# Optimization experiments

Measured on AMD Instinct MI355X. Metric: run time of the kernel, lower is better.

The kernel has to match this reference:

```python
import jax, jax.numpy as jnp
import numpy as np

EPS = 1e-6


def setup_inputs() -> dict:
    key = jax.random.key(0)
    k1, k2, k3, k4, k5, k6, k7 = jax.random.split(key, 7)
    B, S, D, P = 16384, 8, 128, 65536
    return {
        "z_samples": jax.random.normal(k1, (B, S, D), dtype=jnp.float32),
        "alpha": jax.random.normal(k2, (), dtype=jnp.float32),
        "beta": jax.random.normal(k3, (), dtype=jnp.float32),
        "ap": jax.random.randint(k4, (P,), 0, B),
        "p": jax.random.randint(k5, (P,), 0, B),
        "an": jax.random.randint(k6, (P,), 0, B),
        "n": jax.random.randint(k7, (P,), 0, B),
    }


def _pairwise_sqdist(Xa, Xb):
    # Xa, Xb: [P, S, D] -> d2: [P, S, S] where d2[p,i,j] = ||Xa[p,i]-Xb[p,j]||^2
    S = Xa.shape[1]
    rows = []
    for i in range(S):  # S is a small fixed constant (n_samples)
        diff = Xa[:, i, None, :] - Xb  # [P, S, D]
        rows.append(jnp.sum(diff * diff, axis=-1))  # [P, S]
    return jnp.stack(rows, axis=1)  # [P, S, S]


def reference(z_samples, alpha, beta, ap, p, an, n):
    S = z_samples.shape[1]
    a = jax.nn.softplus(alpha)
    d2_pos = _pairwise_sqdist(z_samples[ap], z_samples[p])  # [P, S, S]
    d2_neg = _pairwise_sqdist(z_samples[an], z_samples[n])  # [P, S, S]
    prob_pos = jax.nn.sigmoid(-a * d2_pos + beta) + EPS
    prob_neg = jax.nn.sigmoid(-a * d2_neg + beta) + EPS
    per_pair = jnp.sum(-jnp.log(prob_pos) - jnp.log(1.0 - prob_neg), axis=(1, 2))
    per_pair = per_pair / (S * S)
    return jnp.mean(per_pair)
```

## Files before the change

kernel.cpp:

```cpp
#include <hip/hip_runtime.h>


typedef __attribute__((ext_vector_type(8))) short bf16x8;
typedef __attribute__((ext_vector_type(4))) float f32x4;

#define EPS 1e-6f
#define BLOCK_THREADS 256
#define WAVES_PER_BLOCK (BLOCK_THREADS / 64)

__global__ __launch_bounds__(BLOCK_THREADS) void prep_kernel(
    const float* __restrict__ z,
    unsigned char* __restrict__ zq,
    float* __restrict__ norms,
    int totalChunks, int strideChunks)
{
    const int lane = threadIdx.x & 63;
    const int wv   = threadIdx.x >> 6;
    const int wave = blockIdx.x * WAVES_PER_BLOCK + wv;
    const int rg   = lane >> 4;
    const int part = lane & 15;

    for (int chunk = wave; chunk < totalChunks; chunk += strideChunks) {
        const size_t rowBase = (size_t)chunk * 4;
        const size_t off = rowBase * 128 + (size_t)rg * 128 + (size_t)part * 8;
        const float4* src = (const float4*)(z + off);
        float4 c0 = src[0], c1 = src[1];

        float nrm = 0.0f;
        nrm = fmaf(c0.x, c0.x, nrm); nrm = fmaf(c0.y, c0.y, nrm);
        nrm = fmaf(c0.z, c0.z, nrm); nrm = fmaf(c0.w, c0.w, nrm);
        nrm = fmaf(c1.x, c1.x, nrm); nrm = fmaf(c1.y, c1.y, nrm);
        nrm = fmaf(c1.z, c1.z, nrm); nrm = fmaf(c1.w, c1.w, nrm);

        unsigned d0 = 0, d1 = 0;
        d0 = __builtin_amdgcn_cvt_pk_fp8_f32(c0.x, c0.y, d0, false);
        d0 = __builtin_amdgcn_cvt_pk_fp8_f32(c0.z, c0.w, d0, true);
        d1 = __builtin_amdgcn_cvt_pk_fp8_f32(c1.x, c1.y, d1, false);
        d1 = __builtin_amdgcn_cvt_pk_fp8_f32(c1.z, c1.w, d1, true);
        uint2 pk; pk.x = d0; pk.y = d1;
        *((uint2*)(zq + off)) = pk;

        nrm += __shfl_xor(nrm, 1, 64);
        nrm += __shfl_xor(nrm, 2, 64);
        nrm += __shfl_xor(nrm, 4, 64);
        nrm += __shfl_xor(nrm, 8, 64);
        if (part == 0) norms[rowBase + rg] = nrm;
    }
}

union Frag32 { uint4 u4[2]; long l[4]; };

__device__ __forceinline__ void load_pair_fp8(
    const unsigned char* __restrict__ zq, const float* __restrict__ norms,
    const int* __restrict__ ap, const int* __restrict__ pp,
    const int* __restrict__ an, const int* __restrict__ nn,
    int pr, int rr, int q, bool topA,
    Frag32& fa, Frag32& fb, float& na, float& nb)
{
    const int i0 = ap[pr], i1 = pp[pr], i2 = an[pr], i3 = nn[pr];
    const int ia = topA ? i0 : i2;
    const int ib = topA ? i1 : i3;
    const uint4* pA = (const uint4*)(zq + (size_t)ia * 1024 + rr * 128 + q * 32);
    const uint4* pB = (const uint4*)(zq + (size_t)ib * 1024 + rr * 128 + q * 32);
    fa.u4[0] = pA[0]; fa.u4[1] = pA[1];
    fb.u4[0] = pB[0]; fb.u4[1] = pB[1];
    na = norms[ia * 8 + rr];
    nb = norms[ib * 8 + rr];
}

__device__ __forceinline__ float compute_pair_fp8(
    const Frag32& fa, const Frag32& fb, float na, float nb,
    float a, float b, int q, bool pos_side, float eps_sgn, bool valid)
{
    f32x4 acc = {0.f, 0.f, 0.f, 0.f};
    #pragma unroll
    for (int m = 0; m < 4; ++m)
        acc = __builtin_amdgcn_mfma_f32_16x16x32_fp8_fp8(fa.l[m], fb.l[m], acc, 0, 0, 0);

    float cell = 0.0f;
    #pragma unroll
    for (int reg = 0; reg < 4; ++reg) {
        const int row = q * 4 + reg;
        const float nArow = __shfl(na, row, 64);
        const float d2 = nArow + nb - 2.0f * acc[reg];
        const float t = fmaf(-a, d2, b);
        const float t_adj = pos_side ? -t : t;
        const float s = 1.0f / (1.0f + __expf(t_adj)) + eps_sgn;
        cell += -__logf(s);
    }
    return valid ? cell : 0.0f;
}

__global__ __launch_bounds__(BLOCK_THREADS) void hib_main(
    const unsigned char* __restrict__ zq,
    const float* __restrict__ norms,
    const float* __restrict__ alpha,
    const float* __restrict__ beta,
    const int* __restrict__ ap,
    const int* __restrict__ pp,
    const int* __restrict__ an,
    const int* __restrict__ nn,
    float* __restrict__ out,
    int P, int totalWaves, float scale)
{
    __shared__ float red[WAVES_PER_BLOCK];

    const int lane  = threadIdx.x & 63;
    const int wv    = threadIdx.x >> 6;
    const int gwave = blockIdx.x * WAVES_PER_BLOCK + wv;

    const float a = log1pf(expf(alpha[0]));
    const float b = beta[0];

    const int r  = lane & 15;
    const int q  = lane >> 4;
    const int rr = r & 7;
    const bool topA = (r < 8);
    const bool pos_side = (q < 2);
    const bool valid = (pos_side == topA);
    const float eps_sgn = pos_side ? EPS : -EPS;

    float loss = 0.0f;

    for (int pair = gwave; pair < P; pair += 2 * totalWaves) {
        const int pr0 = __builtin_amdgcn_readfirstlane(pair);
        Frag32 fa0, fb0; float na0, nb0;
        load_pair_fp8(zq, norms, ap, pp, an, nn, pr0, rr, q, topA, fa0, fb0, na0, nb0);

        const int pair1 = pair + totalWaves;
        const bool has1 = pair1 < P;
        Frag32 fa1, fb1; float na1 = 0.f, nb1 = 0.f;
        if (has1) {
            const int pr1 = __builtin_amdgcn_readfirstlane(pair1);
            load_pair_fp8(zq, norms, ap, pp, an, nn, pr1, rr, q, topA, fa1, fb1, na1, nb1);
        }

        loss += compute_pair_fp8(fa0, fb0, na0, nb0, a, b, q, pos_side, eps_sgn, valid);
        if (has1)
            loss += compute_pair_fp8(fa1, fb1, na1, nb1, a, b, q, pos_side, eps_sgn, valid);
    }

    #pragma unroll
    for (int off = 32; off > 0; off >>= 1)
        loss += __shfl_down(loss, off, 64);
    if (lane == 0) red[wv] = loss;
    __syncthreads();
    if (threadIdx.x == 0) {
        float s = 0.0f;
        #pragma unroll
        for (int w = 0; w < WAVES_PER_BLOCK; ++w) s += red[w];
        atomicAdd(out, s * scale);
    }
}

__device__ __forceinline__ unsigned pack2_bf16(float lo, float hi) {
    unsigned ulo = __builtin_bit_cast(unsigned, lo) + 0x8000u;
    unsigned uhi = __builtin_bit_cast(unsigned, hi) + 0x8000u;
    return __builtin_amdgcn_perm(uhi, ulo, 0x07060302);
}

union FragAB { bf16x8 v; unsigned u[4]; };

__device__ __forceinline__ void fill_frag(FragAB& f, float4 c0, float4 c1, float& norm) {
    f.u[0] = pack2_bf16(c0.x, c0.y);
    f.u[1] = pack2_bf16(c0.z, c0.w);
    f.u[2] = pack2_bf16(c1.x, c1.y);
    f.u[3] = pack2_bf16(c1.z, c1.w);
    norm = fmaf(c0.x, c0.x, norm); norm = fmaf(c0.y, c0.y, norm);
    norm = fmaf(c0.z, c0.z, norm); norm = fmaf(c0.w, c0.w, norm);
    norm = fmaf(c1.x, c1.x, norm); norm = fmaf(c1.y, c1.y, norm);
    norm = fmaf(c1.z, c1.z, norm); norm = fmaf(c1.w, c1.w, norm);
}

__global__ __launch_bounds__(BLOCK_THREADS) void hib_fallback(
    const float* __restrict__ z,
    const float* __restrict__ alpha,
    const float* __restrict__ beta,
    const int* __restrict__ ap,
    const int* __restrict__ pp_idx,
    const int* __restrict__ an,
    const int* __restrict__ nn_idx,
    float* __restrict__ out,
    int P, int totalWaves, float scale)
{
    __shared__ float red[WAVES_PER_BLOCK];
    const int lane  = threadIdx.x & 63;
    const int wv    = threadIdx.x >> 6;
    const int gwave = blockIdx.x * WAVES_PER_BLOCK + wv;
    const float a = log1pf(expf(alpha[0]));
    const float b = beta[0];
    const int r = lane & 15;
    const int q = lane >> 4;
    const int rr = r & 7;
    const bool pos_side = (q < 2);
    const bool valid = (pos_side == (r < 8));
    const float eps_sgn = pos_side ? EPS : -EPS;
    float loss = 0.0f;

    for (int pair = gwave; pair < P; pair += totalWaves) {
        const int idxA = (r < 8) ? ap[pair] : an[pair];
        const int idxB = (r < 8) ? pp_idx[pair] : nn_idx[pair];
        const float* rowA = z + (size_t)idxA * 1024 + rr * 128 + q * 8;
        const float* rowB = z + (size_t)idxB * 1024 + rr * 128 + q * 8;
        f32x4 acc = {0.f, 0.f, 0.f, 0.f};
        float na = 0.f, nb = 0.f;
        #pragma unroll
        for (int kb = 0; kb < 4; ++kb) {
            const float4* pa = (const float4*)(rowA + kb * 32);
            const float4* pb = (const float4*)(rowB + kb * 32);
            float4 a0 = pa[0], a1 = pa[1];
            float4 b0 = pb[0], b1 = pb[1];
            FragAB fa, fb;
            fill_frag(fa, a0, a1, na);
            fill_frag(fb, b0, b1, nb);
            acc = __builtin_amdgcn_mfma_f32_16x16x32_bf16(fa.v, fb.v, acc, 0, 0, 0);
        }
        na += __shfl_xor(na, 16, 64);
        na += __shfl_xor(na, 32, 64);
        nb += __shfl_xor(nb, 16, 64);
        nb += __shfl_xor(nb, 32, 64);
        float cell = 0.0f;
        #pragma unroll
        for (int reg = 0; reg < 4; ++reg) {
            const int row = q * 4 + reg;
            const float nArow = __shfl(na, row, 64);
            const float d2 = nArow + nb - 2.0f * acc[reg];
            float t = fmaf(-a, d2, b);
            const float t_adj = pos_side ? -t : t;
            const float s = 1.0f / (1.0f + __expf(t_adj)) + eps_sgn;
            cell += -__logf(s);
        }
        if (valid) loss += cell;
    }

    #pragma unroll
    for (int off = 32; off > 0; off >>= 1)
        loss += __shfl_down(loss, off, 64);
    if (lane == 0) red[wv] = loss;
    __syncthreads();
    if (threadIdx.x == 0) {
        float s = 0.0f;
        #pragma unroll
        for (int w = 0; w < WAVES_PER_BLOCK; ++w) s += red[w];
        atomicAdd(out, s * scale);
    }
}

extern "C" void kernel_launch(void* const* d_in, const int* in_sizes, int n_in,
                              void* d_out, int out_size, void* d_ws, size_t ws_size,
                              hipStream_t stream) {
    const float* z     = (const float*)d_in[0];
    const float* alpha = (const float*)d_in[1];
    const float* beta  = (const float*)d_in[2];
    const int*   ap    = (const int*)d_in[3];
    const int*   p     = (const int*)d_in[4];
    const int*   an    = (const int*)d_in[5];
    const int*   n     = (const int*)d_in[6];
    float* out = (float*)d_out;

    const int P = in_sizes[3];
    const int zElems = in_sizes[0];
    const int totalRows = zElems / 128;

    hipMemsetAsync(out, 0, sizeof(float), stream);

    const int blocks = 4096;
    const int totalWaves = blocks * WAVES_PER_BLOCK;
    const float scale = 1.0f / ((float)P * 64.0f);

    const size_t zqBytes = (size_t)zElems * sizeof(unsigned char);
    const size_t need = zqBytes + (size_t)totalRows * sizeof(float);

    if (ws_size >= need) {
        unsigned char* zq = (unsigned char*)d_ws;
        float* norms = (float*)((char*)d_ws + zqBytes);

        const int totalChunks = totalRows / 4;
        const int prepBlocks = 2048;
        prep_kernel<<<prepBlocks, BLOCK_THREADS, 0, stream>>>(
            z, zq, norms, totalChunks, prepBlocks * WAVES_PER_BLOCK);

        hib_main<<<blocks, BLOCK_THREADS, 0, stream>>>(
            zq, norms, alpha, beta, ap, p, an, n, out, P, totalWaves, scale);
    } else {
        hib_fallback<<<blocks, BLOCK_THREADS, 0, stream>>>(
            z, alpha, beta, ap, p, an, n, out, P, totalWaves, scale);
    }
    (void)n_in; (void)out_size;
}
```

Before: 169.8 us.

## Batch four pairs per wave, permute fp8 layout, and fold logs into products

```diff
diff --git a/kernel.cpp b/kernel.cpp
--- a/kernel.cpp
+++ b/kernel.cpp
@@ -20,9 +20,11 @@
     const int rg   = lane >> 4;
     const int part = lane & 15;
 
+    const int physOff = ((part >> 2) << 4) + (((part >> 1) & 1) << 6) + ((part & 1) << 3);
+
     for (int chunk = wave; chunk < totalChunks; chunk += strideChunks) {
-        const size_t rowBase = (size_t)chunk * 4;
-        const size_t off = rowBase * 128 + (size_t)rg * 128 + (size_t)part * 8;
+        const size_t rowIdx = (size_t)chunk * 4 + rg;
+        const size_t off = rowIdx * 128 + (size_t)part * 8;
         const float4* src = (const float4*)(z + off);
         float4 c0 = src[0], c1 = src[1];
 
@@ -38,57 +40,62 @@
         d1 = __builtin_amdgcn_cvt_pk_fp8_f32(c1.x, c1.y, d1, false);
         d1 = __builtin_amdgcn_cvt_pk_fp8_f32(c1.z, c1.w, d1, true);
         uint2 pk; pk.x = d0; pk.y = d1;
-        *((uint2*)(zq + off)) = pk;
+        *((uint2*)(zq + rowIdx * 128 + physOff)) = pk;
 
         nrm += __shfl_xor(nrm, 1, 64);
         nrm += __shfl_xor(nrm, 2, 64);
         nrm += __shfl_xor(nrm, 4, 64);
         nrm += __shfl_xor(nrm, 8, 64);
-        if (part == 0) norms[rowBase + rg] = nrm;
+        if (part == 0) norms[rowIdx] = nrm;
     }
 }
 
 union Frag32 { uint4 u4[2]; long l[4]; };
 
-__device__ __forceinline__ void load_pair_fp8(
+__device__ __forceinline__ void load_one_pair(
     const unsigned char* __restrict__ zq, const float* __restrict__ norms,
-    const int* __restrict__ ap, const int* __restrict__ pp,
-    const int* __restrict__ an, const int* __restrict__ nn,
-    int pr, int rr, int q, bool topA,
+    int ia, int ib, int rr, int q,
     Frag32& fa, Frag32& fb, float& na, float& nb)
 {
-    const int i0 = ap[pr], i1 = pp[pr], i2 = an[pr], i3 = nn[pr];
-    const int ia = topA ? i0 : i2;
-    const int ib = topA ? i1 : i3;
-    const uint4* pA = (const uint4*)(zq + (size_t)ia * 1024 + rr * 128 + q * 32);
-    const uint4* pB = (const uint4*)(zq + (size_t)ib * 1024 + rr * 128 + q * 32);
-    fa.u4[0] = pA[0]; fa.u4[1] = pA[1];
-    fb.u4[0] = pB[0]; fb.u4[1] = pB[1];
+    const unsigned char* rowA = zq + (size_t)ia * 1024 + rr * 128;
+    const unsigned char* rowB = zq + (size_t)ib * 1024 + rr * 128;
+    fa.u4[0] = *(const uint4*)(rowA + q * 16);
+    fa.u4[1] = *(const uint4*)(rowA + 64 + q * 16);
+    fb.u4[0] = *(const uint4*)(rowB + q * 16);
+    fb.u4[1] = *(const uint4*)(rowB + 64 + q * 16);
     na = norms[ia * 8 + rr];
     nb = norms[ib * 8 + rr];
 }
 
-__device__ __forceinline__ float compute_pair_fp8(
+__device__ __forceinline__ float pair_epilogue(
     const Frag32& fa, const Frag32& fb, float na, float nb,
-    float a, float b, int q, bool pos_side, float eps_sgn, bool valid)
-{
-    f32x4 acc = {0.f, 0.f, 0.f, 0.f};
-    #pragma unroll
-    for (int m = 0; m < 4; ++m)
-        acc = __builtin_amdgcn_mfma_f32_16x16x32_fp8_fp8(fa.l[m], fb.l[m], acc, 0, 0, 0);
-
-    float cell = 0.0f;
+    float a, float negb, int q, float sgn, float eps_sgn, float one_p,
+    float valid_f)
+{
+    f32x4 acc0 = {0.f, 0.f, 0.f, 0.f};
+    f32x4 acc1 = {0.f, 0.f, 0.f, 0.f};
+    acc0 = __builtin_amdgcn_mfma_f32_16x16x32_fp8_fp8(fa.l[0], fb.l[0], acc0, 0, 0, 0);
+    acc1 = __builtin_amdgcn_mfma_f32_16x16x32_fp8_fp8(fa.l[1], fb.l[1], acc1, 0, 0, 0);
+    acc0 = __builtin_amdgcn_mfma_f32_16x16x32_fp8_fp8(fa.l[2], fb.l[2], acc0, 0, 0, 0);
+    acc1 = __builtin_amdgcn_mfma_f32_16x16x32_fp8_fp8(fa.l[3], fb.l[3], acc1, 0, 0, 0);
+    f32x4 acc = acc0 + acc1;
+
+    float den = 1.0f, num = 1.0f;
     #pragma unroll
     for (int reg = 0; reg < 4; ++reg) {
         const int row = q * 4 + reg;
         const float nArow = __shfl(na, row, 64);
-        const float d2 = nArow + nb - 2.0f * acc[reg];
-        const float t = fmaf(-a, d2, b);
-        const float t_adj = pos_side ? -t : t;
-        const float s = 1.0f / (1.0f + __expf(t_adj)) + eps_sgn;
-        cell += -__logf(s);
-    }
-    return valid ? cell : 0.0f;
+        const float ssum = nArow + nb;
+        const float d2 = fmaf(-2.0f, acc[reg], ssum);
+        const float u = fmaf(a, d2, negb);
+        float x = u * sgn;
+        x = fminf(x, 20.0f);
+        const float E = __expf(x);
+        den *= (1.0f + E);
+        num *= fmaf(eps_sgn, E, one_p);
+    }
+    const float pl = __log2f(den) - __log2f(num);
+    return valid_f * pl;
 }
 
 __global__ __launch_bounds__(BLOCK_THREADS) void hib_main(
@@ -101,43 +108,65 @@
     const int* __restrict__ an,
     const int* __restrict__ nn,
     float* __restrict__ out,
-    int P, int totalWaves, float scale)
+    int P, float scale)
 {
     __shared__ float red[WAVES_PER_BLOCK];
 
     const int lane  = threadIdx.x & 63;
     const int wv    = threadIdx.x >> 6;
     const int gwave = blockIdx.x * WAVES_PER_BLOCK + wv;
-
-    const float a = log1pf(expf(alpha[0]));
-    const float b = beta[0];
+    const int pairBase = __builtin_amdgcn_readfirstlane(gwave * 4);
+
+    const float a    = log1pf(expf(alpha[0]));
+    const float negb = -beta[0];
 
     const int r  = lane & 15;
     const int q  = lane >> 4;
     const int rr = r & 7;
     const bool topA = (r < 8);
     const bool pos_side = (q < 2);
-    const bool valid = (pos_side == topA);
+    const float valid_f = (pos_side == topA) ? 1.0f : 0.0f;
+    const float sgn     = pos_side ? 1.0f : -1.0f;
     const float eps_sgn = pos_side ? EPS : -EPS;
+    const float one_p   = 1.0f + eps_sgn;
 
     float loss = 0.0f;
 
-    for (int pair = gwave; pair < P; pair += 2 * totalWaves) {
-        const int pr0 = __builtin_amdgcn_readfirstlane(pair);
-        Frag32 fa0, fb0; float na0, nb0;
-        load_pair_fp8(zq, norms, ap, pp, an, nn, pr0, rr, q, topA, fa0, fb0, na0, nb0);
-
-        const int pair1 = pair + totalWaves;
-        const bool has1 = pair1 < P;
-        Frag32 fa1, fb1; float na1 = 0.f, nb1 = 0.f;
-        if (has1) {
-            const int pr1 = __builtin_amdgcn_readfirstlane(pair1);
-            load_pair_fp8(zq, norms, ap, pp, an, nn, pr1, rr, q, topA, fa1, fb1, na1, nb1);
+    if (pairBase < P) {
+        if (pairBase + 3 < P) {
+            const int4 A4 = *(const int4*)(ap + pairBase);
+            const int4 P4 = *(const int4*)(pp + pairBase);
+            const int4 N4 = *(const int4*)(an + pairBase);
+            const int4 M4 = *(const int4*)(nn + pairBase);
+            const int iap[4] = {A4.x, A4.y, A4.z, A4.w};
+            const int ipp[4] = {P4.x, P4.y, P4.z, P4.w};
+            const int ian[4] = {N4.x, N4.y, N4.z, N4.w};
+            const int inn[4] = {M4.x, M4.y, M4.z, M4.w};
+
+            Frag32 fa[4], fb[4];
+            float na[4], nb[4];
+            #pragma unroll
+            for (int k = 0; k < 4; ++k) {
+                const int ia = topA ? iap[k] : ian[k];
+                const int ib = topA ? ipp[k] : inn[k];
+                load_one_pair(zq, norms, ia, ib, rr, q, fa[k], fb[k], na[k], nb[k]);
+            }
+            #pragma unroll
+            for (int k = 0; k < 4; ++k)
+                loss += pair_epilogue(fa[k], fb[k], na[k], nb[k],
+                                      a, negb, q, sgn, eps_sgn, one_p, valid_f);
+        } else {
+            for (int k = 0; k < 4; ++k) {
+                const int pr = pairBase + k;
+                if (pr >= P) break;
+                const int ia = topA ? ap[pr] : an[pr];
+                const int ib = topA ? pp[pr] : nn[pr];
+                Frag32 fa, fb; float na, nb;
+                load_one_pair(zq, norms, ia, ib, rr, q, fa, fb, na, nb);
+                loss += pair_epilogue(fa, fb, na, nb,
+                                      a, negb, q, sgn, eps_sgn, one_p, valid_f);
+            }
         }
-
-        loss += compute_pair_fp8(fa0, fb0, na0, nb0, a, b, q, pos_side, eps_sgn, valid);
-        if (has1)
-            loss += compute_pair_fp8(fa1, fb1, na1, nb1, a, b, q, pos_side, eps_sgn, valid);
     }
 
     #pragma unroll
@@ -210,10 +239,10 @@
             const float4* pb = (const float4*)(rowB + kb * 32);
             float4 a0 = pa[0], a1 = pa[1];
             float4 b0 = pb[0], b1 = pb[1];
-            FragAB fa, fb;
-            fill_frag(fa, a0, a1, na);
-            fill_frag(fb, b0, b1, nb);
-            acc = __builtin_amdgcn_mfma_f32_16x16x32_bf16(fa.v, fb.v, acc, 0, 0, 0);
+            FragAB fav, fbv;
+            fill_frag(fav, a0, a1, na);
+            fill_frag(fbv, b0, b1, nb);
+            acc = __builtin_amdgcn_mfma_f32_16x16x32_bf16(fav.v, fbv.v, acc, 0, 0, 0);
         }
         na += __shfl_xor(na, 16, 64);
         na += __shfl_xor(na, 32, 64);
@@ -264,10 +293,6 @@
 
     hipMemsetAsync(out, 0, sizeof(float), stream);
 
-    const int blocks = 4096;
-    const int totalWaves = blocks * WAVES_PER_BLOCK;
-    const float scale = 1.0f / ((float)P * 64.0f);
-
     const size_t zqBytes = (size_t)zElems * sizeof(unsigned char);
     const size_t need = zqBytes + (size_t)totalRows * sizeof(float);
 
@@ -280,9 +305,16 @@
         prep_kernel<<<prepBlocks, BLOCK_THREADS, 0, stream>>>(
             z, zq, norms, totalChunks, prepBlocks * WAVES_PER_BLOCK);
 
+        const int totalWaves = (P + 3) / 4;
+        const int blocks = (totalWaves + WAVES_PER_BLOCK - 1) / WAVES_PER_BLOCK;
+        const float scale = 0.6931471805599453f / ((float)P * 64.0f);
+
         hib_main<<<blocks, BLOCK_THREADS, 0, stream>>>(
-            zq, norms, alpha, beta, ap, p, an, n, out, P, totalWaves, scale);
+            zq, norms, alpha, beta, ap, p, an, n, out, P, scale);
     } else {
+        const int blocks = 4096;
+        const int totalWaves = blocks * WAVES_PER_BLOCK;
+        const float scale = 1.0f / ((float)P * 64.0f);
         hib_fallback<<<blocks, BLOCK_THREADS, 0, stream>>>(
             z, alpha, beta, ap, p, an, n, out, P, totalWaves, scale);
     }
```

After: 168.5 us. No clear change (-0.8%).
